# Performance work log

Hardware: AMD Instinct MI355X
Metric: run time of the kernel (lower is better)

## Reference

```python
import jax, jax.numpy as jnp
import numpy as np

T = 256          # n_tokens
APR = 3          # atoms_per_residue
N = T * APR      # n_atoms = 768
CA = 128         # atom_embedding_size
CP = 16          # atom_pair_embedding_size
CT = 384         # token_embedding_size
CS = 384         # single_embedding_size
CZ = 128         # pair_embedding_size
NB = 3           # num_block
H = 4            # num_head
DH = CA // H
NQ = 32          # num_queries (query block size)
NK = 128         # num_keys (local key window)


def _ln(x, g, b):
    m = jnp.mean(x, -1, keepdims=True)
    v = jnp.mean((x - m) ** 2, -1, keepdims=True)
    return (x - m) * jax.lax.rsqrt(v + 1e-5) * g + b


def setup_inputs() -> dict:
    key = jax.random.key(0)
    ks = jax.random.split(key, 32)
    w = lambda k, shape: jax.random.normal(k, shape, jnp.float32) * 0.02
    return {
        "ref_pos": jax.random.normal(ks[0], (N, 3), jnp.float32),
        "ref_space_uid": jax.random.randint(ks[1], (N,), 0, T),
        "r": jax.random.normal(ks[2], (N, 3), jnp.float32),
        "s": jax.random.normal(ks[3], (T, CS), jnp.float32),
        "z": jax.random.normal(ks[4], (T, T, CZ), jnp.float32),
        "W_pos": w(ks[5], (3, CA)),
        "W_pos_offset": w(ks[6], (3, CP)),
        "W_inv_sq_dist": w(ks[7], (1, CP)),
        "W_mask": w(ks[8], (1, CP)),
        "W_cond_a": w(ks[9], (CA, CP)),
        "W_cond_b": w(ks[10], (CA, CP)),
        "ln_s_g": jnp.ones((CS,), jnp.float32), "ln_s_b": jnp.zeros((CS,), jnp.float32),
        "W_single": w(ks[11], (CS, CA)),
        "ln_z_g": jnp.ones((CZ,), jnp.float32), "ln_z_b": jnp.zeros((CZ,), jnp.float32),
        "W_pair": w(ks[12], (CZ, CP)),
        "W_noisy": w(ks[13], (3, CA)),
        "W_mlp1": w(ks[14], (CP, CP)),
        "W_mlp2": w(ks[15], (CP, CP)),
        "W_mlp3": w(ks[16], (CP, CP)),
        "at_ln_g": jnp.ones((NB, CA), jnp.float32), "at_ln_b": jnp.zeros((NB, CA), jnp.float32),
        "at_Wq": w(ks[17], (NB, CA, CA)),
        "at_Wk": w(ks[18], (NB, CA, CA)),
        "at_Wv": w(ks[19], (NB, CA, CA)),
        "at_Wg": w(ks[20], (NB, CA, CA)),
        "at_lnp_g": jnp.ones((NB, CP), jnp.float32), "at_lnp_b": jnp.zeros((NB, CP), jnp.float32),
        "at_Wb": w(ks[21], (NB, CP, H)),
        "at_Wo": w(ks[22], (NB, CA, CA)),
        "at_ln2_g": jnp.ones((NB, CA), jnp.float32), "at_ln2_b": jnp.zeros((NB, CA), jnp.float32),
        "at_Wt1": w(ks[23], (NB, CA, 4 * CA)),
        "at_Wt2": w(ks[24], (NB, 4 * CA, CA)),
        "W_proj": w(ks[25], (CA, CT)),
    }


def _forward(ref_pos, ref_space_uid, r, s, z, W_pos, W_pos_offset, W_inv_sq_dist, W_mask,
             W_cond_a, W_cond_b, ln_s_g, ln_s_b, W_single, ln_z_g, ln_z_b, W_pair, W_noisy,
             W_mlp1, W_mlp2, W_mlp3, at_ln_g, at_ln_b, at_Wq, at_Wk, at_Wv, at_Wg,
             at_lnp_g, at_lnp_b, at_Wb, at_Wo, at_ln2_g, at_ln2_b, at_Wt1, at_Wt2, W_proj):
    c = ref_pos @ W_pos                                             # [N,CA]
    dist = ref_pos[:, None, :] - ref_pos[None, :, :]                # [N,N,3]
    maskf = (ref_space_uid[:, None] == ref_space_uid[None, :])[..., None].astype(jnp.float32)
    pair = (dist @ W_pos_offset) * maskf                            # [N,N,CP]
    sq = jnp.sum(dist * dist, -1, keepdims=True)                    # [N,N,1]
    pair = pair + ((1.0 / (1.0 + sq)) @ W_inv_sq_dist) * maskf
    pair = pair + (maskf @ W_mask) * maskf
    q = c
    # r is not None branch
    c = c + _ln(jnp.tile(s, (APR, 1)), ln_s_g, ln_s_b) @ W_single
    pair = pair + _ln(jnp.tile(z, (APR, APR, 1)), ln_z_g, ln_z_b) @ W_pair
    q = q + r @ W_noisy
    rc = jax.nn.relu(c)
    pair = pair + (rc @ W_cond_a)[:, None, :] + (rc @ W_cond_b)[None, :, :]
    h = jax.nn.relu(pair) @ W_mlp1
    h = jax.nn.relu(h) @ W_mlp2
    h = jax.nn.relu(h) @ W_mlp3
    pair = pair + h
    # sequence-local attention mask (AF3-style: query blocks of NQ attend a NK-wide window)
    idx = jnp.arange(N)
    center = (idx // NQ) * NQ + (NQ - 1) / 2.0
    beta = jnp.where(jnp.abs(idx[None, :].astype(jnp.float32) - center[:, None]) < NK / 2.0, 0.0, -1e9)
    scale = 1.0 / np.sqrt(DH).astype(np.float32)
    x = q
    for b in range(NB):
        a = _ln(x, at_ln_g[b], at_ln_b[b])
        qh = (a @ at_Wq[b]).reshape(N, H, DH)
        kh = (a @ at_Wk[b]).reshape(N, H, DH)
        vh = (a @ at_Wv[b]).reshape(N, H, DH)
        bias = _ln(pair, at_lnp_g[b], at_lnp_b[b]) @ at_Wb[b]       # [N,N,H]
        logits = jnp.einsum('ihd,jhd->hij', qh, kh) * scale + bias.transpose(2, 0, 1) + beta[None]
        attn = jax.nn.softmax(logits, axis=-1)
        o = jnp.einsum('hij,jhd->ihd', attn, vh)
        g = jax.nn.sigmoid(a @ at_Wg[b]).reshape(N, H, DH)
        x = x + (o * g).reshape(N, CA) @ at_Wo[b]
        t = _ln(x, at_ln2_g[b], at_ln2_b[b])
        x = x + jax.nn.relu(t @ at_Wt1[b]) @ at_Wt2[b]
    qout = jax.nn.relu(x @ W_proj)                                  # [N,CT]
    a_out = jnp.mean(qout.reshape(T, APR, CT), axis=-2)             # [T,CT]
    return a_out, qout, c, pair


def reference(ref_pos, ref_space_uid, r, s, z, W_pos, W_pos_offset, W_inv_sq_dist, W_mask,
              W_cond_a, W_cond_b, ln_s_g, ln_s_b, W_single, ln_z_g, ln_z_b, W_pair, W_noisy,
              W_mlp1, W_mlp2, W_mlp3, at_ln_g, at_ln_b, at_Wq, at_Wk, at_Wv, at_Wg,
              at_lnp_g, at_lnp_b, at_Wb, at_Wo, at_ln2_g, at_ln2_b, at_Wt1, at_Wt2, W_proj):
    return _forward(ref_pos, ref_space_uid, r, s, z, W_pos, W_pos_offset, W_inv_sq_dist, W_mask,
                    W_cond_a, W_cond_b, ln_s_g, ln_s_b, W_single, ln_z_g, ln_z_b, W_pair, W_noisy,
                    W_mlp1, W_mlp2, W_mlp3, at_ln_g, at_ln_b, at_Wq, at_Wk, at_Wv, at_Wg,
                    at_lnp_g, at_lnp_b, at_Wb, at_Wo, at_ln2_g, at_ln2_b, at_Wt1, at_Wt2, W_proj)
```

## Files before the change

kernel.cpp:

```cpp
#include <hip/hip_runtime.h>
#include <math.h>


__device__ __forceinline__ float sigmoidf_(float v) { return 1.f / (1.f + __expf(-v)); }

typedef __attribute__((ext_vector_type(4))) short s16x4;
typedef __attribute__((ext_vector_type(8))) short s16x8;
typedef __attribute__((ext_vector_type(4))) float f32x4;

__device__ __forceinline__ unsigned bfpack(float a, float b) {
  return (__float_as_uint(a) >> 16) | (__float_as_uint(b) & 0xFFFF0000u);
}
__device__ __forceinline__ short bf1(float a) { return (short)(__float_as_uint(a) >> 16); }

__global__ __launch_bounds__(256) void k_front(
    const float* __restrict__ z, const float* __restrict__ zg,
    const float* __restrict__ zlb, const float* __restrict__ W_pair,
    float* __restrict__ zp,
    const float* __restrict__ s, const float* __restrict__ g,
    const float* __restrict__ b, const float* __restrict__ W_single,
    const float* __restrict__ ref_pos, const float* __restrict__ r,
    const float* __restrict__ W_pos, const float* __restrict__ W_noisy,
    const float* __restrict__ Wca, const float* __restrict__ Wcb,
    float* __restrict__ c_out, float* __restrict__ x,
    float* __restrict__ ca, float* __restrict__ cb) {
  __shared__ __align__(128) float sm[5392];
  int t = threadIdx.x;
  int bid = blockIdx.x;
  if (bid < 1024) {
    float* bcp = sm + 5120;
    float* Bc = sm + 5376;
    {
      int ch = t & 15, kseg = t >> 4;
      float a = 0.f;
#pragma unroll
      for (int e = 0; e < 8; e++) {
        int k = kseg * 8 + e;
        a += zlb[k] * W_pair[k * 16 + ch];
      }
      bcp[kseg * 16 + ch] = a;
    }
    __syncthreads();
    if (t < 16) {
      float a = 0.f;
#pragma unroll
      for (int kseg = 0; kseg < 16; kseg++) a += bcp[kseg * 16 + t];
      Bc[t] = a;
    }
    __syncthreads();
    int w = t >> 6, l = t & 63;
    int kb = l & 15, rg = l >> 4;
    int row0 = bid * 64 + w * 16;
    char* stgw = (char*)(sm + w * 1280);
    float4 za[4], zb[4];
    float m_[4], rs_[4];
#pragma unroll
    for (int rr = 0; rr < 4; rr++) {
      long base = (long)(row0 + rg * 4 + rr) * 128 + kb * 8;
      za[rr] = *(const float4*)&z[base];
      zb[rr] = *(const float4*)&z[base + 4];
      float ps = za[rr].x + za[rr].y + za[rr].z + za[rr].w +
                 zb[rr].x + zb[rr].y + zb[rr].z + zb[rr].w;
      float pq = za[rr].x * za[rr].x + za[rr].y * za[rr].y + za[rr].z * za[rr].z +
                 za[rr].w * za[rr].w + zb[rr].x * zb[rr].x + zb[rr].y * zb[rr].y +
                 zb[rr].z * zb[rr].z + zb[rr].w * zb[rr].w;
#pragma unroll
      for (int o = 1; o < 16; o <<= 1) { ps += __shfl_xor(ps, o); pq += __shfl_xor(pq, o); }
      m_[rr] = ps * (1.f / 128.f);
      rs_[rr] = rsqrtf(pq * (1.f / 128.f) - m_[rr] * m_[rr] + 1e-5f);
    }
    {
      int kc = kb >> 1;
      int cbase = (kb & 1) * 8;
#pragma unroll
      for (int e = 0; e < 8; e++) {
        float a0 = ((e < 4 ? (&za[0].x)[e] : (&zb[0].x)[e - 4]) - m_[0]) * rs_[0];
        float a1 = ((e < 4 ? (&za[1].x)[e] : (&zb[1].x)[e - 4]) - m_[1]) * rs_[1];
        float a2 = ((e < 4 ? (&za[2].x)[e] : (&zb[2].x)[e - 4]) - m_[2]) * rs_[2];
        float a3 = ((e < 4 ? (&za[3].x)[e] : (&zb[3].x)[e - 4]) - m_[3]) * rs_[3];
        char* wp = stgw + kc * 640 + (cbase + e) * 32 + rg * 8;
        *(uint2*)wp = make_uint2(bfpack(a0, a1), bfpack(a2, a3));
      }
    }
    int c = l & 15;
    s16x8 bw[8];
#pragma unroll
    for (int kc = 0; kc < 8; kc++) {
      short e0, e1, e2, e3;
      {
        int kk = kc * 16 + 4 * rg;
        e0 = bf1(zg[kk] * W_pair[kk * 16 + c]);
        e1 = bf1(zg[kk + 1] * W_pair[(kk + 1) * 16 + c]);
        e2 = bf1(zg[kk + 2] * W_pair[(kk + 2) * 16 + c]);
        e3 = bf1(zg[kk + 3] * W_pair[(kk + 3) * 16 + c]);
      }
      bw[kc] = s16x8{e0, e1, e2, e3, (short)0, (short)0, (short)0, (short)0};
    }
    unsigned sbase = (unsigned)(uintptr_t)stgw;
    f32x4 acc = {0.f, 0.f, 0.f, 0.f};
#pragma unroll
    for (int kc = 0; kc < 8; kc++) {
      unsigned ra = sbase + (unsigned)(kc * 640 + c * 8 + rg * 128);
      s16x4 tr;
      asm volatile("s_waitcnt lgkmcnt(0)\n\tds_read_b64_tr_b16 %0, %1\n\ts_waitcnt lgkmcnt(0)"
                   : "=v"(tr) : "v"(ra) : "memory");
      s16x8 a8 = {tr[0], tr[1], tr[2], tr[3], (short)0, (short)0, (short)0, (short)0};
      acc = __builtin_amdgcn_mfma_f32_16x16x32_bf16(a8, bw[kc], acc, 0, 0, 0);
    }
    float bc = Bc[c];
#pragma unroll
    for (int rr = 0; rr < 4; rr++) {
      int row = row0 + rg * 4 + rr;
      zp[(long)row * 16 + c] = acc[rr] + bc;
    }
  } else {
    int tok = bid - 1024;
    float* sln = sm;
    float* ws = sm + 384;
    float* red = sm + 4480;
    float* rc = sm + 4488;
    float v0 = 0.f, v1 = 0.f, v2 = 0.f;
    if (t < 128) {
      v0 = s[tok * 384 + t]; v1 = s[tok * 384 + 128 + t]; v2 = s[tok * 384 + 256 + t];
      float ps = v0 + v1 + v2, pq = v0 * v0 + v1 * v1 + v2 * v2;
#pragma unroll
      for (int o = 1; o < 64; o <<= 1) { ps += __shfl_xor(ps, o); pq += __shfl_xor(pq, o); }
      if ((t & 63) == 0) { red[t >> 6] = ps; red[2 + (t >> 6)] = pq; }
    }
    __syncthreads();
    float ctv = 0.f;
    if (t < 128) {
      float mean = (red[0] + red[1]) * (1.f / 384.f);
      float var = (red[2] + red[3]) * (1.f / 384.f) - mean * mean;
      float rstd = rsqrtf(var + 1e-5f);
      sln[t] = (v0 - mean) * rstd * g[t] + b[t];
      sln[128 + t] = (v1 - mean) * rstd * g[128 + t] + b[128 + t];
      sln[256 + t] = (v2 - mean) * rstd * g[256 + t] + b[256 + t];
    }
    for (int c0 = 0; c0 < 384; c0 += 32) {
      __syncthreads();
#pragma unroll
      for (int m = 0; m < 4; m++) {
        int idx = (t + 256 * m) * 4;
        *(float4*)&ws[idx] = *(const float4*)&W_single[c0 * 128 + idx];
      }
      __syncthreads();
      if (t < 128) {
#pragma unroll 8
        for (int kk = 0; kk < 32; kk++) ctv += sln[c0 + kk] * ws[kk * 128 + t];
      }
    }
    float wp0 = 0.f, wp1 = 0.f, wp2 = 0.f, wn0 = 0.f, wn1 = 0.f, wn2 = 0.f;
    if (t < 128) {
      wp0 = W_pos[t]; wp1 = W_pos[128 + t]; wp2 = W_pos[256 + t];
      wn0 = W_noisy[t]; wn1 = W_noisy[128 + t]; wn2 = W_noisy[256 + t];
    }
#pragma unroll
    for (int a = 0; a < 3; a++) {
      int i = tok + 256 * a;
      float cc = 0.f;
      if (t < 128) {
        float p0 = ref_pos[i * 3], p1 = ref_pos[i * 3 + 1], p2 = ref_pos[i * 3 + 2];
        float r0 = r[i * 3], r1 = r[i * 3 + 1], r2 = r[i * 3 + 2];
        float c0 = p0 * wp0 + p1 * wp1 + p2 * wp2;
        x[i * 128 + t] = c0 + r0 * wn0 + r1 * wn1 + r2 * wn2;
        cc = c0 + ctv;
        c_out[i * 128 + t] = cc;
      }
      __syncthreads();
      if (t < 128) rc[t] = fmaxf(cc, 0.f);
      __syncthreads();
      if (t < 128) {
        int out_id = t >> 2, q = t & 3;
        const float* Wm = (out_id < 16) ? Wca : Wcb;
        int ch = out_id & 15;
        float acc = 0.f;
#pragma unroll
        for (int kk = 0; kk < 32; kk++) { int k = q * 32 + kk; acc += rc[k] * Wm[k * 16 + ch]; }
        acc += __shfl_xor(acc, 1);
        acc += __shfl_xor(acc, 2);
        if (q == 0) { if (out_id < 16) ca[i * 16 + ch] = acc; else cb[i * 16 + ch] = acc; }
      }
    }
  }
}

__global__ __launch_bounds__(256) void k_pairq(
    const float* __restrict__ ref_pos, const int* __restrict__ uid,
    const float* __restrict__ Wpo, const float* __restrict__ Wisd,
    const float* __restrict__ Wmask, const float* __restrict__ W1,
    const float* __restrict__ W2, const float* __restrict__ W3,
    const float* __restrict__ zp, const float* __restrict__ ca,
    const float* __restrict__ cb, const float* __restrict__ lnp_g,
    const float* __restrict__ lnp_b, const float* __restrict__ Wb,
    float* __restrict__ pair_out, float* __restrict__ biasA,
    const float* __restrict__ x, const float* __restrict__ lng,
    const float* __restrict__ lnb, const float* __restrict__ Wq,
    const float* __restrict__ Wk, const float* __restrict__ Wv,
    const float* __restrict__ Wg, float* __restrict__ qkvg) {
  __shared__ float jsx[256], jsy[256], jsz[256];
  __shared__ int jsu[256];
  __shared__ __align__(128) short stg[4][1280];
  __shared__ __align__(16) float pfs[4][1056];
  __shared__ float wgb[192];
  __shared__ float kbs[12];
  int t = threadIdx.x;
  int bid = blockIdx.x;
  if (bid >= 2304) {
    int r0 = (bid - 2304) * 2;
    float* asr_ = jsx;
    float* red_ = jsy;
    int row = t >> 7, c = t & 127;
    float xv = x[(r0 + row) * 128 + c];
    {
      float ps = xv, pq = xv * xv;
#pragma unroll
      for (int o = 1; o < 64; o <<= 1) { ps += __shfl_xor(ps, o); pq += __shfl_xor(pq, o); }
      int wv = t >> 6;
      if ((t & 63) == 0) { red_[wv] = ps; red_[4 + wv] = pq; }
      __syncthreads();
      float mean = (red_[2 * row] + red_[2 * row + 1]) * (1.f / 128.f);
      float var = (red_[4 + 2 * row] + red_[4 + 2 * row + 1]) * (1.f / 128.f) - mean * mean;
      float rstd = rsqrtf(var + 1e-5f);
      asr_[row * 128 + c] = (xv - mean) * rstd * lng[c] + lnb[c];
    }
    __syncthreads();
    {
      int c4 = (t & 127) * 4, row2 = t >> 7;
      int mtx = c4 >> 7, lc = c4 & 127;
      const float* Wm = (mtx == 0) ? Wq : (mtx == 1) ? Wk : (mtx == 2) ? Wv : Wg;
      float a0 = 0.f, a1 = 0.f, a2 = 0.f, a3 = 0.f;
#pragma unroll 8
      for (int k = 0; k < 128; k++) {
        float4 w = *(const float4*)&Wm[k * 128 + lc];
        float av = asr_[row2 * 128 + k];
        a0 += av * w.x; a1 += av * w.y; a2 += av * w.z; a3 += av * w.w;
      }
      *(float4*)&qkvg[(r0 + row2) * 512 + c4] = make_float4(a0, a1, a2, a3);
    }
    return;
  }
  int i = bid / 3, jb = bid % 3;
  int jg = jb * 256 + t;
  jsx[t] = ref_pos[jg * 3];
  jsy[t] = ref_pos[jg * 3 + 1];
  jsz[t] = ref_pos[jg * 3 + 2];
  jsu[t] = uid[jg];
  if (t >= 64) {
    int e = t - 64;
    if (e < 192) {
      int bq = e >> 6, k = (e >> 2) & 15, h = e & 3;
      wgb[e] = lnp_g[bq * 16 + k] * Wb[bq * 64 + k * 4 + h];
    }
  }
  if (t >= 48 && t < 60) {
    int e = t - 48, bq = e >> 2, h = e & 3;
    float a = 0.f;
#pragma unroll
    for (int cc = 0; cc < 16; cc++) a += lnp_b[bq * 16 + cc] * Wb[bq * 64 + cc * 4 + h];
    kbs[e] = a;
  }
  int w = t >> 6, l = t & 63;
  int c = l & 15, gr = l >> 4;
  float pix = ref_pos[i * 3], piy = ref_pos[i * 3 + 1], piz = ref_pos[i * 3 + 2];
  int ui = uid[i];
  float w0c = Wpo[c], w1c = Wpo[16 + c], w2c = Wpo[32 + c];
  float wic = Wisd[c], wmc = Wmask[c], cac = ca[i * 16 + c];
  s16x8 bw0 = {bf1(W1[(4 * gr + 0) * 16 + c]), bf1(W1[(4 * gr + 1) * 16 + c]),
               bf1(W1[(4 * gr + 2) * 16 + c]), bf1(W1[(4 * gr + 3) * 16 + c]),
               (short)0, (short)0, (short)0, (short)0};
  s16x8 bw1 = {bf1(W2[(4 * gr + 0) * 16 + c]), bf1(W2[(4 * gr + 1) * 16 + c]),
               bf1(W2[(4 * gr + 2) * 16 + c]), bf1(W2[(4 * gr + 3) * 16 + c]),
               (short)0, (short)0, (short)0, (short)0};
  s16x8 bw2 = {bf1(W3[(4 * gr + 0) * 16 + c]), bf1(W3[(4 * gr + 1) * 16 + c]),
               bf1(W3[(4 * gr + 2) * 16 + c]), bf1(W3[(4 * gr + 3) * 16 + c]),
               (short)0, (short)0, (short)0, (short)0};
  __syncthreads();
  char* sb = (char*)&stg[w][0];
  unsigned sbase = (unsigned)(uintptr_t)sb;
  f32x4 z4 = {0.f, 0.f, 0.f, 0.f};
#pragma unroll
  for (int g = 0; g < 4; g++) {
    float p0_, p1_, p2_, p3_;
    {
      int jl0 = w * 64 + g * 16 + 4 * gr;
#pragma unroll
      for (int r = 0; r < 4; r++) {
        int jloc = jl0 + r;
        int j = jb * 256 + jloc;
        float d0 = pix - jsx[jloc], d1 = piy - jsy[jloc], d2 = piz - jsz[jloc];
        float mk = (ui == jsu[jloc]) ? 1.f : 0.f;
        float inv = 1.f / (1.f + d0 * d0 + d1 * d1 + d2 * d2);
        float zv = zp[((long)((i & 255) << 8) + jloc) * 16 + c];
        float cbv = cb[j * 16 + c];
        float pv = mk * (d0 * w0c + d1 * w1c + d2 * w2c + inv * wic + wmc) + zv + cbv + cac;
        if (r == 0) p0_ = pv; else if (r == 1) p1_ = pv; else if (r == 2) p2_ = pv; else p3_ = pv;
      }
    }
    char* wp = sb + g * 640 + c * 32 + gr * 8;
    unsigned ra = sbase + (unsigned)(g * 640 + c * 8 + gr * 128);
    *(uint2*)wp = make_uint2(bfpack(fmaxf(p0_, 0.f), fmaxf(p1_, 0.f)),
                             bfpack(fmaxf(p2_, 0.f), fmaxf(p3_, 0.f)));
    s16x4 tr0;
    asm volatile("s_waitcnt lgkmcnt(0)\n\tds_read_b64_tr_b16 %0, %1\n\ts_waitcnt lgkmcnt(0)"
                 : "=v"(tr0) : "v"(ra) : "memory");
    s16x8 a8 = {tr0[0], tr0[1], tr0[2], tr0[3], (short)0, (short)0, (short)0, (short)0};
    f32x4 h1 = __builtin_amdgcn_mfma_f32_16x16x32_bf16(a8, bw0, z4, 0, 0, 0);
    *(uint2*)wp = make_uint2(bfpack(fmaxf(h1[0], 0.f), fmaxf(h1[1], 0.f)),
                             bfpack(fmaxf(h1[2], 0.f), fmaxf(h1[3], 0.f)));
    s16x4 tr1;
    asm volatile("s_waitcnt lgkmcnt(0)\n\tds_read_b64_tr_b16 %0, %1\n\ts_waitcnt lgkmcnt(0)"
                 : "=v"(tr1) : "v"(ra) : "memory");
    s16x8 a8b = {tr1[0], tr1[1], tr1[2], tr1[3], (short)0, (short)0, (short)0, (short)0};
    f32x4 h2 = __builtin_amdgcn_mfma_f32_16x16x32_bf16(a8b, bw1, z4, 0, 0, 0);
    *(uint2*)wp = make_uint2(bfpack(fmaxf(h2[0], 0.f), fmaxf(h2[1], 0.f)),
                             bfpack(fmaxf(h2[2], 0.f), fmaxf(h2[3], 0.f)));
    s16x4 tr2;
    asm volatile("s_waitcnt lgkmcnt(0)\n\tds_read_b64_tr_b16 %0, %1\n\ts_waitcnt lgkmcnt(0)"
                 : "=v"(tr2) : "v"(ra) : "memory");
    s16x8 a8c = {tr2[0], tr2[1], tr2[2], tr2[3], (short)0, (short)0, (short)0, (short)0};
    f32x4 h3 = __builtin_amdgcn_mfma_f32_16x16x32_bf16(a8c, bw2, z4, 0, 0, 0);
    float f0 = p0_ + h3[0], f1 = p1_ + h3[1], f2 = p2_ + h3[2], f3 = p3_ + h3[3];
    {
      int jl0 = w * 64 + g * 16 + 4 * gr;
      long pb = ((long)i * 768 + (long)(jb * 256 + jl0)) * 16 + c;
      pair_out[pb] = f0;
      pair_out[pb + 16] = f1;
      pair_out[pb + 32] = f2;
      pair_out[pb + 48] = f3;
    }
    *(float4*)&pfs[w][g * 264 + c * 16 + 4 * gr] = make_float4(f0, f1, f2, f3);
  }
  asm volatile("s_waitcnt lgkmcnt(0)" ::: "memory");
  int qb = i >> 5;
  int j = jb * 256 + t;
  unsigned jw = (unsigned)(j - (qb * 32 - 48));
  if (jw < 128u) {
    int gt = (t >> 4) & 3, jr = t & 15;
    float v[16];
#pragma unroll
    for (int cc = 0; cc < 16; cc++) v[cc] = pfs[w][gt * 264 + cc * 16 + jr];
    float m = 0.f;
#pragma unroll
    for (int cc = 0; cc < 16; cc++) m += v[cc];
    m *= (1.f / 16.f);
    float vv = 0.f;
#pragma unroll
    for (int cc = 0; cc < 16; cc++) { float d = v[cc] - m; vv += d * d; }
    float rs = rsqrtf(vv * (1.f / 16.f) + 1e-5f);
    float nrm[16];
#pragma unroll
    for (int cc = 0; cc < 16; cc++) nrm[cc] = (v[cc] - m) * rs;
    int qi = i & 31;
#pragma unroll
    for (int bq = 0; bq < 3; bq++) {
      float o0 = kbs[bq * 4 + 0], o1 = kbs[bq * 4 + 1];
      float o2 = kbs[bq * 4 + 2], o3 = kbs[bq * 4 + 3];
#pragma unroll
      for (int k = 0; k < 16; k++) {
        float nv = nrm[k];
        float4 wv = *(float4*)&wgb[bq * 64 + k * 4];
        o0 += nv * wv.x; o1 += nv * wv.y; o2 += nv * wv.z; o3 += nv * wv.w;
      }
      long base = (long)(bq * 96 + qb * 4) * 4096 + (long)qi * 128 + jw;
      biasA[base] = o0;
      biasA[base + 4096] = o1;
      biasA[base + 2 * 4096] = o2;
      biasA[base + 3 * 4096] = o3;
    }
  }
}

__global__ __launch_bounds__(256) void k_attn2(
    const float* __restrict__ qkvg, const float* __restrict__ biasb,
    float* __restrict__ og) {
  int qt = blockIdx.x >> 2, h = blockIdx.x & 3, t = threadIdx.x;
  int i0 = qt * 16;
  int qb32 = qt >> 1;
  int lo = qb32 * 32 - 48;
  int qoff = (qt & 1) * 16;
  __shared__ float qs[16][36];
  __shared__ float ks[128][36];
  __shared__ float vs[128][36];
  __shared__ float L[16][132];
  {
    int e = t * 8;
    int qi = e >> 7, k8 = e & 127;
    const float* bb = &biasb[(long)(qb32 * 4 + h) * 4096 + (long)(qoff + qi) * 128];
#pragma unroll
    for (int m = 0; m < 2; m++) {
      int k4 = k8 + m * 4;
      int j4 = lo + k4;
      float4 bv;
      if (j4 >= 0 && j4 <= 764) bv = *(const float4*)&bb[k4];
      else bv = make_float4(-1e30f, -1e30f, -1e30f, -1e30f);
      *(float4*)&L[qi][k4] = bv;
    }
  }
  if (t < 128) {
    int qi = t >> 3, dq = (t & 7) * 4;
    *(float4*)&qs[qi][dq] = *(const float4*)&qkvg[(i0 + qi) * 512 + h * 32 + dq];
  }
  {
    int kj = t >> 1, dh = (t & 1) * 16;
    int j = lo + kj;
    if (j >= 0 && j < 768) {
      const float4* sk = (const float4*)&qkvg[j * 512 + 128 + h * 32 + dh];
      const float4* sv = (const float4*)&qkvg[j * 512 + 256 + h * 32 + dh];
#pragma unroll
      for (int m = 0; m < 4; m++) {
        *(float4*)&ks[kj][dh + 4 * m] = sk[m];
        *(float4*)&vs[kj][dh + 4 * m] = sv[m];
      }
    } else {
      float4 zz = {0, 0, 0, 0};
#pragma unroll
      for (int m = 0; m < 4; m++) {
        *(float4*)&ks[kj][dh + 4 * m] = zz;
        *(float4*)&vs[kj][dh + 4 * m] = zz;
      }
    }
  }
  __syncthreads();
  const float scale = 0.17677669529663687f;
  {
    int qi = t & 15, kb = t >> 4;
    float4 qr[8];
#pragma unroll
    for (int m = 0; m < 8; m++) qr[m] = *(float4*)&qs[qi][m * 4];
#pragma unroll
    for (int kk = 0; kk < 8; kk++) {
      int kj = kb * 8 + kk;
      float acc = 0.f;
#pragma unroll
      for (int m = 0; m < 8; m++) {
        float4 kv = *(float4*)&ks[kj][m * 4];
        acc += qr[m].x * kv.x + qr[m].y * kv.y + qr[m].z * kv.z + qr[m].w * kv.w;
      }
      L[qi][kj] += acc * scale;
    }
  }
  __syncthreads();
  int qi = t >> 4, sg = t & 15;
  float mx = -1e30f;
#pragma unroll
  for (int k2 = 0; k2 < 8; k2++) mx = fmaxf(mx, L[qi][sg * 8 + k2]);
#pragma unroll
  for (int o = 1; o < 16; o <<= 1) mx = fmaxf(mx, __shfl_xor(mx, o));
  float sum = 0.f;
#pragma unroll
  for (int k2 = 0; k2 < 8; k2++) {
    int kj = sg * 8 + k2;
    float e = __expf(L[qi][kj] - mx);
    L[qi][kj] = e;
    sum += e;
  }
#pragma unroll
  for (int o = 1; o < 16; o <<= 1) sum += __shfl_xor(sum, o);
  float rden = 1.f / sum;
  __syncthreads();
  {
    int d2 = (t & 15) * 2;
    float a0 = 0.f, a1 = 0.f;
#pragma unroll 8
    for (int kj = 0; kj < 128; kj++) {
      float p = L[qi][kj];
      float2 v = *(float2*)&vs[kj][d2];
      a0 += p * v.x; a1 += p * v.y;
    }
    int i = i0 + qi;
    float2 gr = *(const float2*)&qkvg[i * 512 + 384 + h * 32 + d2];
    float2 o2;
    o2.x = a0 * rden * sigmoidf_(gr.x);
    o2.y = a1 * rden * sigmoidf_(gr.y);
    *(float2*)&og[i * 128 + h * 32 + d2] = o2;
  }
}

template <int MODE>
__global__ __launch_bounds__(384) void k_fusedT(
    const float* __restrict__ og, const float* __restrict__ Wo,
    const float* __restrict__ g2, const float* __restrict__ b2,
    const float* __restrict__ Wt1, const float* __restrict__ Wt2,
    float* __restrict__ x,
    const float* __restrict__ lng_n, const float* __restrict__ lnb_n,
    const float* __restrict__ Wq, const float* __restrict__ Wk,
    const float* __restrict__ Wv, const float* __restrict__ Wg,
    float* __restrict__ qkvg, const float* __restrict__ W_proj,
    float* __restrict__ out) {
  int t = threadIdx.x;
  int r0 = blockIdx.x * 3;
  __shared__ float osr[3][128];
  __shared__ float xns[3][128];
  __shared__ float asr[3][128];
  __shared__ float hs[3][512];
  __shared__ float part[4][3][128];
  __shared__ float red[12];
  {
    int rr = t >> 7, c = t & 127;
    osr[rr][c] = og[(r0 + rr) * 128 + c];
    xns[rr][c] = x[(r0 + rr) * 128 + c];
  }
  __syncthreads();
  {
    int c4 = (t & 31) * 4, row = (t >> 5) % 3, q = t / 96;
    int k0 = q * 32;
    float a0 = 0.f, a1 = 0.f, a2 = 0.f, a3 = 0.f;
#pragma unroll 8
    for (int kk = 0; kk < 32; kk++) {
      int k = k0 + kk;
      float4 w = *(const float4*)&Wo[k * 128 + c4];
      float av = osr[row][k];
      a0 += av * w.x; a1 += av * w.y; a2 += av * w.z; a3 += av * w.w;
    }
    *(float4*)&part[q][row][c4] = make_float4(a0, a1, a2, a3);
  }
  __syncthreads();
  {
    int rr = t >> 7, c = t & 127;
    float xv = xns[rr][c] + part[0][rr][c] + part[1][rr][c] + part[2][rr][c] + part[3][rr][c];
    float ps = xv, pq = xv * xv;
#pragma unroll
    for (int o = 1; o < 64; o <<= 1) { ps += __shfl_xor(ps, o); pq += __shfl_xor(pq, o); }
    int wv = t >> 6;
    if ((t & 63) == 0) { red[wv] = ps; red[6 + wv] = pq; }
    __syncthreads();
    float mean = (red[2 * rr] + red[2 * rr + 1]) * (1.f / 128.f);
    float var = (red[6 + 2 * rr] + red[6 + 2 * rr + 1]) * (1.f / 128.f) - mean * mean;
    float rstd = rsqrtf(var + 1e-5f);
    xns[rr][c] = xv;
    asr[rr][c] = (xv - mean) * rstd * g2[c] + b2[c];
  }
  __syncthreads();
  {
    int c4 = (t & 127) * 4, row = t >> 7;
    float a0 = 0.f, a1 = 0.f, a2 = 0.f, a3 = 0.f;
#pragma unroll 8
    for (int k = 0; k < 128; k++) {
      float4 w = *(const float4*)&Wt1[k * 512 + c4];
      float av = asr[row][k];
      a0 += av * w.x; a1 += av * w.y; a2 += av * w.z; a3 += av * w.w;
    }
    *(float4*)&hs[row][c4] = make_float4(fmaxf(a0, 0.f), fmaxf(a1, 0.f),
                                         fmaxf(a2, 0.f), fmaxf(a3, 0.f));
  }
  __syncthreads();
  {
    int c4 = (t & 31) * 4, row = (t >> 5) % 3, q = t / 96;
    int k0 = q * 128;
    float a0 = 0.f, a1 = 0.f, a2 = 0.f, a3 = 0.f;
#pragma unroll 8
    for (int kk = 0; kk < 128; kk++) {
      int k = k0 + kk;
      float4 w = *(const float4*)&Wt2[k * 128 + c4];
      float hv = hs[row][k];
      a0 += hv * w.x; a1 += hv * w.y; a2 += hv * w.z; a3 += hv * w.w;
    }
    *(float4*)&part[q][row][c4] = make_float4(a0, a1, a2, a3);
  }
  __syncthreads();
  {
    int rr = t >> 7, c = t & 127;
    float xf = xns[rr][c] + part[0][rr][c] + part[1][rr][c] +
               part[2][rr][c] + part[3][rr][c];
    x[(r0 + rr) * 128 + c] = xf;
    xns[rr][c] = xf;
  }
  if (MODE == 1) {
    __syncthreads();
    {
      int rr = t >> 7, c = t & 127;
      float xv = xns[rr][c];
      float ps = xv, pq = xv * xv;
#pragma unroll
      for (int o = 1; o < 64; o <<= 1) { ps += __shfl_xor(ps, o); pq += __shfl_xor(pq, o); }
      int wv = t >> 6;
      if ((t & 63) == 0) { red[wv] = ps; red[6 + wv] = pq; }
      __syncthreads();
      float mean = (red[2 * rr] + red[2 * rr + 1]) * (1.f / 128.f);
      float var = (red[6 + 2 * rr] + red[6 + 2 * rr + 1]) * (1.f / 128.f) - mean * mean;
      float rstd = rsqrtf(var + 1e-5f);
      asr[rr][c] = (xv - mean) * rstd * lng_n[c] + lnb_n[c];
    }
    __syncthreads();
    {
      int c4 = (t & 127) * 4, row = t >> 7;
      int mtx = c4 >> 7, lc = c4 & 127;
      const float* Wm = (mtx == 0) ? Wq : (mtx == 1) ? Wk : (mtx == 2) ? Wv : Wg;
      float a0 = 0.f, a1 = 0.f, a2 = 0.f, a3 = 0.f;
#pragma unroll 8
      for (int k = 0; k < 128; k++) {
        float4 w = *(const float4*)&Wm[k * 128 + lc];
        float av = asr[row][k];
        a0 += av * w.x; a1 += av * w.y; a2 += av * w.z; a3 += av * w.w;
      }
      *(float4*)&qkvg[(r0 + row) * 512 + c4] = make_float4(a0, a1, a2, a3);
    }
  }
  if (MODE == 2) {
    __syncthreads();
    int tk = blockIdx.x;
    float a0 = 0.f, a1 = 0.f, a2 = 0.f;
#pragma unroll 8
    for (int k = 0; k < 128; k++) {
      float w = W_proj[k * 384 + t];
      a0 += xns[0][k] * w; a1 += xns[1][k] * w; a2 += xns[2][k] * w;
    }
    a0 = fmaxf(a0, 0.f); a1 = fmaxf(a1, 0.f); a2 = fmaxf(a2, 0.f);
    out[98304 + (tk * 3 + 0) * 384 + t] = a0;
    out[98304 + (tk * 3 + 1) * 384 + t] = a1;
    out[98304 + (tk * 3 + 2) * 384 + t] = a2;
    out[tk * 384 + t] = (a0 + a1 + a2) * (1.f / 3.f);
  }
}

extern "C" void kernel_launch(void* const* d_in, const int* in_sizes, int n_in,
                              void* d_out, int out_size, void* d_ws, size_t ws_size,
                              hipStream_t stream) {
  const float* ref_pos  = (const float*)d_in[0];
  const int*   uid      = (const int*)d_in[1];
  const float* r        = (const float*)d_in[2];
  const float* s        = (const float*)d_in[3];
  const float* z        = (const float*)d_in[4];
  const float* W_pos    = (const float*)d_in[5];
  const float* Wpo      = (const float*)d_in[6];
  const float* Wisd     = (const float*)d_in[7];
  const float* Wmask    = (const float*)d_in[8];
  const float* Wca      = (const float*)d_in[9];
  const float* Wcb      = (const float*)d_in[10];
  const float* ln_s_g   = (const float*)d_in[11];
  const float* ln_s_b   = (const float*)d_in[12];
  const float* W_single = (const float*)d_in[13];
  const float* ln_z_g   = (const float*)d_in[14];
  const float* ln_z_b   = (const float*)d_in[15];
  const float* W_pair   = (const float*)d_in[16];
  const float* W_noisy  = (const float*)d_in[17];
  const float* W_mlp1   = (const float*)d_in[18];
  const float* W_mlp2   = (const float*)d_in[19];
  const float* W_mlp3   = (const float*)d_in[20];
  const float* at_ln_g  = (const float*)d_in[21];
  const float* at_ln_b  = (const float*)d_in[22];
  const float* at_Wq    = (const float*)d_in[23];
  const float* at_Wk    = (const float*)d_in[24];
  const float* at_Wv    = (const float*)d_in[25];
  const float* at_Wg    = (const float*)d_in[26];
  const float* at_lnp_g = (const float*)d_in[27];
  const float* at_lnp_b = (const float*)d_in[28];
  const float* at_Wb    = (const float*)d_in[29];
  const float* at_Wo    = (const float*)d_in[30];
  const float* at_ln2_g = (const float*)d_in[31];
  const float* at_ln2_b = (const float*)d_in[32];
  const float* at_Wt1   = (const float*)d_in[33];
  const float* at_Wt2   = (const float*)d_in[34];
  const float* W_proj   = (const float*)d_in[35];
  float* out = (float*)d_out;
  float* W = (float*)d_ws;
  float* x     = W;
  float* ca    = W + 98304;
  float* cb    = W + 110592;
  float* zp    = W + 122880;
  float* biasA = W + 1171456;
  float* qkvg  = W + 2351104;
  float* og    = W + 2744320;

  k_front<<<1280, 256, 0, stream>>>(z, ln_z_g, ln_z_b, W_pair, zp,
                                    s, ln_s_g, ln_s_b, W_single, ref_pos, r,
                                    W_pos, W_noisy, Wca, Wcb,
                                    out + 393216, x, ca, cb);
  k_pairq<<<2688, 256, 0, stream>>>(ref_pos, uid, Wpo, Wisd, Wmask, W_mlp1, W_mlp2,
                                    W_mlp3, zp, ca, cb, at_lnp_g, at_lnp_b, at_Wb,
                                    out + 491520, biasA,
                                    x, at_ln_g, at_ln_b, at_Wq, at_Wk, at_Wv, at_Wg,
                                    qkvg);
  k_attn2<<<192, 256, 0, stream>>>(qkvg, biasA, og);
  k_fusedT<1><<<256, 384, 0, stream>>>(og, at_Wo, at_ln2_g, at_ln2_b, at_Wt1, at_Wt2, x,
                                       at_ln_g + 128, at_ln_b + 128,
                                       at_Wq + 16384, at_Wk + 16384,
                                       at_Wv + 16384, at_Wg + 16384, qkvg,
                                       nullptr, nullptr);
  k_attn2<<<192, 256, 0, stream>>>(qkvg, biasA + 393216, og);
  k_fusedT<1><<<256, 384, 0, stream>>>(og, at_Wo + 16384, at_ln2_g + 128, at_ln2_b + 128,
                                       at_Wt1 + 65536, at_Wt2 + 65536, x,
                                       at_ln_g + 256, at_ln_b + 256,
                                       at_Wq + 32768, at_Wk + 32768,
                                       at_Wv + 32768, at_Wg + 32768, qkvg,
                                       nullptr, nullptr);
  k_attn2<<<192, 256, 0, stream>>>(qkvg, biasA + 786432, og);
  k_fusedT<2><<<256, 384, 0, stream>>>(og, at_Wo + 32768, at_ln2_g + 256, at_ln2_b + 256,
                                       at_Wt1 + 131072, at_Wt2 + 131072, x,
                                       nullptr, nullptr, nullptr, nullptr,
                                       nullptr, nullptr, nullptr, W_proj, out);
}
```

Measured before the change: 145.3 us.

## Widen fused transition kernel to 512 threads with split-K GEMVs reusing weights across rows

The fused transition kernel now launches 512 threads. Its Wt1, Wt2 and QKVG matrix-vector stages are restructured so each thread loads a weight float4 once and applies it to all three rows, with the K dimension split across thread groups and partial sums reduced through a new shared buffer. This is meant to cut redundant weight loads from global memory and shorten each thread's serial K loop. In exchange it adds shared memory for the partials, extra barriers and reduction passes, and leaves 128 threads idle in the row-wise phases.

```diff
diff --git a/kernel.cpp b/kernel.cpp
--- a/kernel.cpp
+++ b/kernel.cpp
@@ -478,7 +478,7 @@
 }
 
 template <int MODE>
-__global__ __launch_bounds__(384) void k_fusedT(
+__global__ __launch_bounds__(512) void k_fusedT(
     const float* __restrict__ og, const float* __restrict__ Wo,
     const float* __restrict__ g2, const float* __restrict__ b2,
     const float* __restrict__ Wt1, const float* __restrict__ Wt2,
@@ -495,14 +495,15 @@
   __shared__ float asr[3][128];
   __shared__ float hs[3][512];
   __shared__ float part[4][3][128];
+  __shared__ float part2[4][3][512];
   __shared__ float red[12];
-  {
+  if (t < 384) {
     int rr = t >> 7, c = t & 127;
     osr[rr][c] = og[(r0 + rr) * 128 + c];
     xns[rr][c] = x[(r0 + rr) * 128 + c];
   }
   __syncthreads();
-  {
+  if (t < 384) {
     int c4 = (t & 31) * 4, row = (t >> 5) % 3, q = t / 96;
     int k0 = q * 32;
     float a0 = 0.f, a1 = 0.f, a2 = 0.f, a3 = 0.f;
@@ -516,7 +517,7 @@
     *(float4*)&part[q][row][c4] = make_float4(a0, a1, a2, a3);
   }
   __syncthreads();
-  {
+  if (t < 384) {
     int rr = t >> 7, c = t & 127;
     float xv = xns[rr][c] + part[0][rr][c] + part[1][rr][c] + part[2][rr][c] + part[3][rr][c];
     float ps = xv, pq = xv * xv;
@@ -524,7 +525,11 @@
     for (int o = 1; o < 64; o <<= 1) { ps += __shfl_xor(ps, o); pq += __shfl_xor(pq, o); }
     int wv = t >> 6;
     if ((t & 63) == 0) { red[wv] = ps; red[6 + wv] = pq; }
-    __syncthreads();
+  }
+  __syncthreads();
+  if (t < 384) {
+    int rr = t >> 7, c = t & 127;
+    float xv = xns[rr][c] + part[0][rr][c] + part[1][rr][c] + part[2][rr][c] + part[3][rr][c];
     float mean = (red[2 * rr] + red[2 * rr + 1]) * (1.f / 128.f);
     float var = (red[6 + 2 * rr] + red[6 + 2 * rr + 1]) * (1.f / 128.f) - mean * mean;
     float rstd = rsqrtf(var + 1e-5f);
@@ -533,42 +538,67 @@
   }
   __syncthreads();
   {
-    int c4 = (t & 127) * 4, row = t >> 7;
-    float a0 = 0.f, a1 = 0.f, a2 = 0.f, a3 = 0.f;
+    int cg4 = (t & 127) * 4, ks = t >> 7;
+    int k0 = ks * 32;
+    float a00 = 0.f, a01 = 0.f, a02 = 0.f, a03 = 0.f;
+    float a10 = 0.f, a11 = 0.f, a12 = 0.f, a13 = 0.f;
+    float a20 = 0.f, a21 = 0.f, a22 = 0.f, a23 = 0.f;
 #pragma unroll 8
-    for (int k = 0; k < 128; k++) {
-      float4 w = *(const float4*)&Wt1[k * 512 + c4];
-      float av = asr[row][k];
-      a0 += av * w.x; a1 += av * w.y; a2 += av * w.z; a3 += av * w.w;
-    }
-    *(float4*)&hs[row][c4] = make_float4(fmaxf(a0, 0.f), fmaxf(a1, 0.f),
-                                         fmaxf(a2, 0.f), fmaxf(a3, 0.f));
+    for (int kk = 0; kk < 32; kk++) {
+      int k = k0 + kk;
+      float4 w = *(const float4*)&Wt1[k * 512 + cg4];
+      float v0 = asr[0][k], v1 = asr[1][k], v2 = asr[2][k];
+      a00 += v0 * w.x; a01 += v0 * w.y; a02 += v0 * w.z; a03 += v0 * w.w;
+      a10 += v1 * w.x; a11 += v1 * w.y; a12 += v1 * w.z; a13 += v1 * w.w;
+      a20 += v2 * w.x; a21 += v2 * w.y; a22 += v2 * w.z; a23 += v2 * w.w;
+    }
+    *(float4*)&part2[ks][0][cg4] = make_float4(a00, a01, a02, a03);
+    *(float4*)&part2[ks][1][cg4] = make_float4(a10, a11, a12, a13);
+    *(float4*)&part2[ks][2][cg4] = make_float4(a20, a21, a22, a23);
   }
   __syncthreads();
   {
-    int c4 = (t & 31) * 4, row = (t >> 5) % 3, q = t / 96;
-    int k0 = q * 128;
-    float a0 = 0.f, a1 = 0.f, a2 = 0.f, a3 = 0.f;
+#pragma unroll
+    for (int row = 0; row < 3; row++) {
+      float v = part2[0][row][t] + part2[1][row][t] + part2[2][row][t] + part2[3][row][t];
+      hs[row][t] = fmaxf(v, 0.f);
+    }
+  }
+  __syncthreads();
+  {
+    int cg4 = (t & 31) * 4, ks = t >> 5;
+    int k0 = ks * 32;
+    float a00 = 0.f, a01 = 0.f, a02 = 0.f, a03 = 0.f;
+    float a10 = 0.f, a11 = 0.f, a12 = 0.f, a13 = 0.f;
+    float a20 = 0.f, a21 = 0.f, a22 = 0.f, a23 = 0.f;
 #pragma unroll 8
-    for (int kk = 0; kk < 128; kk++) {
+    for (int kk = 0; kk < 32; kk++) {
       int k = k0 + kk;
-      float4 w = *(const float4*)&Wt2[k * 128 + c4];
-      float hv = hs[row][k];
-      a0 += hv * w.x; a1 += hv * w.y; a2 += hv * w.z; a3 += hv * w.w;
-    }
-    *(float4*)&part[q][row][c4] = make_float4(a0, a1, a2, a3);
-  }
-  __syncthreads();
-  {
+      float4 w = *(const float4*)&Wt2[k * 128 + cg4];
+      float v0 = hs[0][k], v1 = hs[1][k], v2 = hs[2][k];
+      a00 += v0 * w.x; a01 += v0 * w.y; a02 += v0 * w.z; a03 += v0 * w.w;
+      a10 += v1 * w.x; a11 += v1 * w.y; a12 += v1 * w.z; a13 += v1 * w.w;
+      a20 += v2 * w.x; a21 += v2 * w.y; a22 += v2 * w.z; a23 += v2 * w.w;
+    }
+    float* p3 = &part2[0][0][0];
+    *(float4*)&p3[(ks * 3 + 0) * 128 + cg4] = make_float4(a00, a01, a02, a03);
+    *(float4*)&p3[(ks * 3 + 1) * 128 + cg4] = make_float4(a10, a11, a12, a13);
+    *(float4*)&p3[(ks * 3 + 2) * 128 + cg4] = make_float4(a20, a21, a22, a23);
+  }
+  __syncthreads();
+  if (t < 384) {
     int rr = t >> 7, c = t & 127;
-    float xf = xns[rr][c] + part[0][rr][c] + part[1][rr][c] +
-               part[2][rr][c] + part[3][rr][c];
+    const float* p3 = &part2[0][0][0];
+    float acc = 0.f;
+#pragma unroll
+    for (int ks = 0; ks < 16; ks++) acc += p3[(ks * 3 + rr) * 128 + c];
+    float xf = xns[rr][c] + acc;
     x[(r0 + rr) * 128 + c] = xf;
     xns[rr][c] = xf;
   }
+  __syncthreads();
   if (MODE == 1) {
-    __syncthreads();
-    {
+    if (t < 384) {
       int rr = t >> 7, c = t & 127;
       float xv = xns[rr][c];
       float ps = xv, pq = xv * xv;
@@ -576,7 +606,11 @@
       for (int o = 1; o < 64; o <<= 1) { ps += __shfl_xor(ps, o); pq += __shfl_xor(pq, o); }
       int wv = t >> 6;
       if ((t & 63) == 0) { red[wv] = ps; red[6 + wv] = pq; }
-      __syncthreads();
+    }
+    __syncthreads();
+    if (t < 384) {
+      int rr = t >> 7, c = t & 127;
+      float xv = xns[rr][c];
       float mean = (red[2 * rr] + red[2 * rr + 1]) * (1.f / 128.f);
       float var = (red[6 + 2 * rr] + red[6 + 2 * rr + 1]) * (1.f / 128.f) - mean * mean;
       float rstd = rsqrtf(var + 1e-5f);
@@ -584,33 +618,50 @@
     }
     __syncthreads();
     {
-      int c4 = (t & 127) * 4, row = t >> 7;
-      int mtx = c4 >> 7, lc = c4 & 127;
+      int cg4 = (t & 127) * 4, ks = t >> 7;
+      int k0 = ks * 32;
+      int mtx = cg4 >> 7, lc = cg4 & 127;
       const float* Wm = (mtx == 0) ? Wq : (mtx == 1) ? Wk : (mtx == 2) ? Wv : Wg;
-      float a0 = 0.f, a1 = 0.f, a2 = 0.f, a3 = 0.f;
+      float a00 = 0.f, a01 = 0.f, a02 = 0.f, a03 = 0.f;
+      float a10 = 0.f, a11 = 0.f, a12 = 0.f, a13 = 0.f;
+      float a20 = 0.f, a21 = 0.f, a22 = 0.f, a23 = 0.f;
+#pragma unroll 8
+      for (int kk = 0; kk < 32; kk++) {
+        int k = k0 + kk;
+        float4 w = *(const float4*)&Wm[k * 128 + lc];
+        float v0 = asr[0][k], v1 = asr[1][k], v2 = asr[2][k];
+        a00 += v0 * w.x; a01 += v0 * w.y; a02 += v0 * w.z; a03 += v0 * w.w;
+        a10 += v1 * w.x; a11 += v1 * w.y; a12 += v1 * w.z; a13 += v1 * w.w;
+        a20 += v2 * w.x; a21 += v2 * w.y; a22 += v2 * w.z; a23 += v2 * w.w;
+      }
+      *(float4*)&part2[ks][0][cg4] = make_float4(a00, a01, a02, a03);
+      *(float4*)&part2[ks][1][cg4] = make_float4(a10, a11, a12, a13);
+      *(float4*)&part2[ks][2][cg4] = make_float4(a20, a21, a22, a23);
+    }
+    __syncthreads();
+    {
+#pragma unroll
+      for (int row = 0; row < 3; row++) {
+        float v = part2[0][row][t] + part2[1][row][t] + part2[2][row][t] + part2[3][row][t];
+        qkvg[(r0 + row) * 512 + t] = v;
+      }
+    }
+  }
+  if (MODE == 2) {
+    if (t < 384) {
+      int tk = blockIdx.x;
+      float a0 = 0.f, a1 = 0.f, a2 = 0.f;
 #pragma unroll 8
       for (int k = 0; k < 128; k++) {
-        float4 w = *(const float4*)&Wm[k * 128 + lc];
-        float av = asr[row][k];
-        a0 += av * w.x; a1 += av * w.y; a2 += av * w.z; a3 += av * w.w;
-      }
-      *(float4*)&qkvg[(r0 + row) * 512 + c4] = make_float4(a0, a1, a2, a3);
-    }
-  }
-  if (MODE == 2) {
-    __syncthreads();
-    int tk = blockIdx.x;
-    float a0 = 0.f, a1 = 0.f, a2 = 0.f;
-#pragma unroll 8
-    for (int k = 0; k < 128; k++) {
-      float w = W_proj[k * 384 + t];
-      a0 += xns[0][k] * w; a1 += xns[1][k] * w; a2 += xns[2][k] * w;
-    }
-    a0 = fmaxf(a0, 0.f); a1 = fmaxf(a1, 0.f); a2 = fmaxf(a2, 0.f);
-    out[98304 + (tk * 3 + 0) * 384 + t] = a0;
-    out[98304 + (tk * 3 + 1) * 384 + t] = a1;
-    out[98304 + (tk * 3 + 2) * 384 + t] = a2;
-    out[tk * 384 + t] = (a0 + a1 + a2) * (1.f / 3.f);
+        float w = W_proj[k * 384 + t];
+        a0 += xns[0][k] * w; a1 += xns[1][k] * w; a2 += xns[2][k] * w;
+      }
+      a0 = fmaxf(a0, 0.f); a1 = fmaxf(a1, 0.f); a2 = fmaxf(a2, 0.f);
+      out[98304 + (tk * 3 + 0) * 384 + t] = a0;
+      out[98304 + (tk * 3 + 1) * 384 + t] = a1;
+      out[98304 + (tk * 3 + 2) * 384 + t] = a2;
+      out[tk * 384 + t] = (a0 + a1 + a2) * (1.f / 3.f);
+    }
   }
 }
 
@@ -673,20 +724,20 @@
                                     x, at_ln_g, at_ln_b, at_Wq, at_Wk, at_Wv, at_Wg,
                                     qkvg);
   k_attn2<<<192, 256, 0, stream>>>(qkvg, biasA, og);
-  k_fusedT<1><<<256, 384, 0, stream>>>(og, at_Wo, at_ln2_g, at_ln2_b, at_Wt1, at_Wt2, x,
+  k_fusedT<1><<<256, 512, 0, stream>>>(og, at_Wo, at_ln2_g, at_ln2_b, at_Wt1, at_Wt2, x,
                                        at_ln_g + 128, at_ln_b + 128,
                                        at_Wq + 16384, at_Wk + 16384,
                                        at_Wv + 16384, at_Wg + 16384, qkvg,
                                        nullptr, nullptr);
   k_attn2<<<192, 256, 0, stream>>>(qkvg, biasA + 393216, og);
-  k_fusedT<1><<<256, 384, 0, stream>>>(og, at_Wo + 16384, at_ln2_g + 128, at_ln2_b + 128,
+  k_fusedT<1><<<256, 512, 0, stream>>>(og, at_Wo + 16384, at_ln2_g + 128, at_ln2_b + 128,
                                        at_Wt1 + 65536, at_Wt2 + 65536, x,
                                        at_ln_g + 256, at_ln_b + 256,
                                        at_Wq + 32768, at_Wk + 32768,
                                        at_Wv + 32768, at_Wg + 32768, qkvg,
                                        nullptr, nullptr);
   k_attn2<<<192, 256, 0, stream>>>(qkvg, biasA + 786432, og);
-  k_fusedT<2><<<256, 384, 0, stream>>>(og, at_Wo + 32768, at_ln2_g + 256, at_ln2_b + 256,
+  k_fusedT<2><<<256, 512, 0, stream>>>(og, at_Wo + 32768, at_ln2_g + 256, at_ln2_b + 256,
                                        at_Wt1 + 131072, at_Wt2 + 131072, x,
                                        nullptr, nullptr, nullptr, nullptr,
                                        nullptr, nullptr, nullptr, W_proj, out);
```

Measured after the change: 143.3 us, median of 2. No clear change (-1.4%).
